# Optimization experiments

Measured on AMD Instinct MI355X. Metric: run time of the kernel, lower is better.

## Reference

```python
import jax, jax.numpy as jnp
import numpy as np

NUM_POINTS = 100000
BATCH = 4096
K = 10


def setup_inputs() -> dict:
    key = jax.random.key(0)
    k1, k2, k3, k4, k5 = jax.random.split(key, 5)
    rays_o = jax.random.normal(k1, (BATCH, 3), dtype=jnp.float32)
    rays_d = jax.random.normal(k2, (BATCH, 3), dtype=jnp.float32)
    xyz = jax.random.normal(k3, (NUM_POINTS, 3), dtype=jnp.float32) * 0.1
    features_dc = jax.random.normal(k4, (NUM_POINTS, 1, 3), dtype=jnp.float32)
    opacity = jax.random.normal(k5, (NUM_POINTS, 1), dtype=jnp.float32)
    return {"rays_o": rays_o, "rays_d": rays_d, "xyz": xyz,
            "features_dc": features_dc, "opacity": opacity}


def reference(rays_o, rays_d, xyz, features_dc, opacity):
    # colors = sigmoid(features[:,0,:]) ; features[:,0,:] == features_dc[:,0,:]
    colors = jax.nn.sigmoid(features_dc[:, 0, :])          # [N,3]
    op = jax.nn.sigmoid(opacity[:, 0])                      # [N]
    ray_centers = rays_o + rays_d * 3.0                     # [B,3]
    # Euclidean cdist via ||a||^2 + ||b||^2 - 2 a.b (matmul form, like torch.cdist p=2)
    sq = (jnp.sum(ray_centers * ray_centers, axis=1)[:, None]
          + jnp.sum(xyz * xyz, axis=1)[None, :]
          - 2.0 * ray_centers @ xyz.T)                      # [B,N]
    distances = jnp.sqrt(jnp.maximum(sq, 0.0))
    # top-K smallest distances per ray
    _, idx = jax.lax.top_k(-distances, K)                   # [B,K]
    d_sel = jnp.take_along_axis(distances, idx, axis=1)     # [B,K]
    w = jnp.exp(-d_sel * 0.1) * op[idx]                     # [B,K]
    w = w / (jnp.sum(w, axis=1, keepdims=True) + 1e-8)
    rgb = jnp.einsum('bk,bkc->bc', w, colors[idx])          # [B,3]
    return rgb
```

## Files before the change

### kernel.cpp

```cpp
#include <hip/hip_runtime.h>
#include <math.h>

#define NPTS   100000
#define NRAYS  4096
#define KTOP   10
#define KMER   12
#define CAP    128
#define LCAP   12

#define PPAIR  2
#define SBLK   98
#define RCS    64
#define RPBS   (NRAYS / RCS)

#define TPAIR  4
#define NPART  64
#define TRAYS  4
#define TGRP   16

typedef float v2f __attribute__((ext_vector_type(2)));

static_assert(SBLK * 1024 >= NPTS, "scan covers all points");
static_assert(TGRP * 2048 <= NPTS, "theta sample within real points");

__device__ __forceinline__ float4 make_center(const float* __restrict__ ro,
                                              const float* __restrict__ rd,
                                              int ray, float w) {
    float ox = ro[3 * ray + 0], oy = ro[3 * ray + 1], oz = ro[3 * ray + 2];
    float dx = rd[3 * ray + 0], dy = rd[3 * ray + 1], dz = rd[3 * ray + 2];
    float cx, cy, cz;
    {
#pragma clang fp contract(off)
        cx = ox + dx * 3.0f;
        cy = oy + dy * 3.0f;
        cz = oz + dz * 3.0f;
    }
    return make_float4(cx, cy, cz, w);
}

__device__ __forceinline__ float sigm(float x) { return 1.0f / (1.0f + expf(-x)); }

__device__ __forceinline__ float rfl(float x) {
    return __int_as_float(__builtin_amdgcn_readfirstlane(__float_as_int(x)));
}

__device__ __forceinline__ v2f score2(v2f px, v2f py, v2f pz, v2f pw,
                                      v2f rx, v2f ry, v2f rz) {
    v2f t = __builtin_elementwise_fma(pz, rz, pw);
    t = __builtin_elementwise_fma(py, ry, t);
    return __builtin_elementwise_fma(px, rx, t);
}

__device__ __forceinline__ unsigned long long mkkey(float sc, int id, bool v) {
    unsigned u = __float_as_uint(sc);
    u = (u & 0x80000000u) ? ~u : (u | 0x80000000u);
    unsigned long long k = ((unsigned long long)u << 32) | (unsigned)(~id);
    return v ? k : 0ull;
}

__global__ __launch_bounds__(256, 3) void theta_kernel(const float* __restrict__ xyz,
                                                       const float* __restrict__ ro,
                                                       const float* __restrict__ rd,
                                                       float4* __restrict__ c4,
                                                       int* __restrict__ cnt) {
    __shared__ float4 rsh[TRAYS];
    __shared__ float  Msh[4][TRAYS][64];
    const int tid = threadIdx.x, wave = tid >> 6, lane = tid & 63;
    const int rbase = blockIdx.x * TRAYS;

    if (tid < TRAYS) rsh[tid] = make_center(ro, rd, rbase + tid, 0.0f);
    __syncthreads();

    float4 rr[TRAYS];
#pragma unroll
    for (int r = 0; r < TRAYS; ++r) rr[r] = rsh[r];

    v2f M[TRAYS];
#pragma unroll
    for (int r = 0; r < TRAYS; ++r) M[r] = (v2f){-INFINITY, -INFINITY};

    v2f pxA[TPAIR], pyA[TPAIR], pzA[TPAIR], pwA[TPAIR];
    v2f pxB[TPAIR], pyB[TPAIR], pzB[TPAIR], pwB[TPAIR];

    auto loadg = [&](v2f* PX, v2f* PY, v2f* PZ, v2f* PW, int g) {
        const int id0 = g * 2048 + wave * 512 + lane;
#pragma unroll
        for (int u = 0; u < TPAIR; ++u) {
            int ia = id0 + (2 * u) * 64, ib = id0 + (2 * u + 1) * 64;
            float xa = xyz[3 * ia + 0], ya = xyz[3 * ia + 1], za = xyz[3 * ia + 2];
            float xb = xyz[3 * ib + 0], yb = xyz[3 * ib + 1], zb = xyz[3 * ib + 2];
            PX[u] = (v2f){xa, xb}; PY[u] = (v2f){ya, yb}; PZ[u] = (v2f){za, zb};
            PW[u] = (v2f){-0.5f * fmaf(xa, xa, fmaf(ya, ya, za * za)),
                          -0.5f * fmaf(xb, xb, fmaf(yb, yb, zb * zb))};
        }
    };
    auto computeg = [&](const v2f* PX, const v2f* PY, const v2f* PZ, const v2f* PW) {
#pragma unroll
        for (int r = 0; r < TRAYS; ++r) {
            const v2f rx = (v2f){rr[r].x, rr[r].x};
            const v2f ry = (v2f){rr[r].y, rr[r].y};
            const v2f rz = (v2f){rr[r].z, rr[r].z};
            v2f m = M[r];
#pragma unroll
            for (int u = 0; u < TPAIR; ++u)
                m = __builtin_elementwise_max(m, score2(PX[u], PY[u], PZ[u], PW[u], rx, ry, rz));
            M[r] = m;
        }
    };

    loadg(pxA, pyA, pzA, pwA, 0);
#pragma unroll 1
    for (int g = 0; g < TGRP; g += 2) {
        loadg(pxB, pyB, pzB, pwB, g + 1);
        computeg(pxA, pyA, pzA, pwA);
        if (g + 2 < TGRP) loadg(pxA, pyA, pzA, pwA, g + 2);
        computeg(pxB, pyB, pzB, pwB);
    }

#pragma unroll
    for (int r = 0; r < TRAYS; ++r)
        Msh[wave][r][lane] = fmaxf(M[r].x, M[r].y);
    __syncthreads();

    if (tid < TRAYS) {
        float vs[KTOP];
#pragma unroll
        for (int j = 0; j < KTOP; ++j) vs[j] = -INFINITY;
#pragma unroll 1
        for (int p = 0; p < NPART; ++p) {
            float v = fmaxf(fmaxf(Msh[0][tid][p], Msh[1][tid][p]),
                            fmaxf(Msh[2][tid][p], Msh[3][tid][p]));
#pragma unroll
            for (int t = KTOP - 1; t >= 1; --t) {
                bool up = v > vs[t - 1], here = v > vs[t];
                vs[t] = up ? vs[t - 1] : (here ? v : vs[t]);
            }
            vs[0] = fmaxf(vs[0], v);
        }
        float4 c = rsh[tid];
        c.w = vs[KTOP - 1];
        c4[rbase + tid] = c;
        cnt[rbase + tid] = 0;
    }
}

__global__ __launch_bounds__(256, 6) void scan_kernel(const float* __restrict__ xyz,
                                                      const float4* __restrict__ c4,
                                                      int* __restrict__ cnt,
                                                      float2* __restrict__ cand) {
    __shared__ int    lcnt[RPBS];
    __shared__ float2 lbuf[RPBS][LCAP];
    const int pblk = blockIdx.x, rchunk = blockIdx.y;
    const int tid = threadIdx.x, wave = tid >> 6, lane = tid & 63;
    const int rbase = rchunk * RPBS;

    if (tid < RPBS) lcnt[tid] = 0;

    const int id0 = pblk * 1024 + wave * 256 + lane;
    v2f px[PPAIR], py[PPAIR], pz[PPAIR], pw[PPAIR];
#pragma unroll
    for (int u = 0; u < PPAIR; ++u) {
        int ia = id0 + (2 * u) * 64, ib = id0 + (2 * u + 1) * 64;
        bool va = ia < NPTS, vb = ib < NPTS;
        int ca = va ? ia : 0, cb = vb ? ib : 0;
        float xa = xyz[3 * ca + 0], ya = xyz[3 * ca + 1], za = xyz[3 * ca + 2];
        float xb = xyz[3 * cb + 0], yb = xyz[3 * cb + 1], zb = xyz[3 * cb + 2];
        px[u] = (v2f){xa, xb}; py[u] = (v2f){ya, yb}; pz[u] = (v2f){za, zb};
        pw[u] = (v2f){va ? -0.5f * fmaf(xa, xa, fmaf(ya, ya, za * za)) : -INFINITY,
                      vb ? -0.5f * fmaf(xb, xb, fmaf(yb, yb, zb * zb)) : -INFINITY};
    }
    __syncthreads();

    auto emit = [&](int r, float sc, int id) {
        int slot = atomicAdd(&lcnt[r], 1);
        float2 e = make_float2(sc, __int_as_float(id));
        if (slot < LCAP) lbuf[r][slot] = e;
        else {
            int gs = atomicAdd(&cnt[rbase + r], 1);
            if (gs < CAP) cand[((rbase + r) << 7) + gs] = e;
        }
    };

    auto do_ray = [&](int r, float cx, float cy, float cz, float th) {
        const v2f rx = (v2f){cx, cx}, ry = (v2f){cy, cy}, rz = (v2f){cz, cz};
        v2f t0 = score2(px[0], py[0], pz[0], pw[0], rx, ry, rz);
        v2f t1 = score2(px[1], py[1], pz[1], pw[1], rx, ry, rz);
        float hm = fmaxf(fmaxf(t0.x, t0.y), fmaxf(t1.x, t1.y));

        if (__ballot(hm >= th)) {
            if (t0.x >= th) emit(r, t0.x, id0 + 0 * 64);
            if (t0.y >= th) emit(r, t0.y, id0 + 1 * 64);
            if (t1.x >= th) emit(r, t1.x, id0 + 2 * 64);
            if (t1.y >= th) emit(r, t1.y, id0 + 3 * 64);
        }
    };

    float qx[4], qy[4], qz[4], qw[4];
    float nx[4], ny[4], nz[4], nw[4];
#pragma unroll
    for (int j = 0; j < 4; ++j) {
        float4 t = c4[rbase + j];
        qx[j] = rfl(t.x); qy[j] = rfl(t.y); qz[j] = rfl(t.z); qw[j] = rfl(t.w);
    }
#pragma unroll 1
    for (int rb = 0; rb < RPBS; rb += 4) {
        const bool more = (rb + 4 < RPBS);
        if (more) {
#pragma unroll
            for (int j = 0; j < 4; ++j) {
                float4 t = c4[rbase + rb + 4 + j];
                nx[j] = rfl(t.x); ny[j] = rfl(t.y); nz[j] = rfl(t.z); nw[j] = rfl(t.w);
            }
        }
#pragma unroll
        for (int j = 0; j < 4; ++j) do_ray(rb + j, qx[j], qy[j], qz[j], qw[j]);
        if (more) {
#pragma unroll
            for (int j = 0; j < 4; ++j) { qx[j] = nx[j]; qy[j] = ny[j]; qz[j] = nz[j]; qw[j] = nw[j]; }
        }
    }

    __syncthreads();
    if (tid < RPBS) {
        int n = lcnt[tid];
        n = n < LCAP ? n : LCAP;
        if (n > 0) {
            const int rayid = rbase + tid;
            int base = atomicAdd(&cnt[rayid], n);
            for (int j = 0; j < n; ++j) {
                int slot = base + j;
                if (slot < CAP) cand[(rayid << 7) + slot] = lbuf[tid][j];
            }
        }
    }
}

__global__ __launch_bounds__(256) void merge_kernel(const float* __restrict__ ro,
                                                    const float* __restrict__ rd,
                                                    const int* __restrict__ cnt,
                                                    const float2* __restrict__ cand,
                                                    const float* __restrict__ xyz,
                                                    const float* __restrict__ fdc,
                                                    const float* __restrict__ opac,
                                                    float* __restrict__ out) {
    const int wave = threadIdx.x >> 6, lane = threadIdx.x & 63;
    const int ray = blockIdx.x * 4 + wave;

    int n = cnt[ray];
    n = n < CAP ? n : CAP;

    const float2* cl = cand + (ray << 7);
    float2 e0 = cl[lane];
    float2 e1 = cl[64 + lane];
    int id0 = __float_as_int(e0.y), id1 = __float_as_int(e1.y);

    unsigned long long k0 = mkkey(e0.x, id0, lane < n);
    unsigned long long k1 = mkkey(e1.x, id1, lane + 64 < n);

    int sel = -1;
    unsigned long long kl = k0 > k1 ? k0 : k1;
#pragma unroll
    for (int j = 0; j < KMER; ++j) {
        unsigned long long m = kl;
#pragma unroll
        for (int off = 1; off < 64; off <<= 1) {
            unsigned long long o = __shfl_xor(m, off);
            m = m > o ? m : o;
        }
        bool win = (kl == m) && (m != 0ull);
        int wid = (k0 >= k1) ? id0 : id1;
        unsigned long long wmask = __ballot(win);
        int wl = __ffsll(wmask) - 1;
        int bid = __shfl(wid, wl & 63);
        if (m == 0ull) bid = -1;
        if (lane == j) sel = bid;
        if (win) {
            if (k0 >= k1) k0 = 0ull; else k1 = 0ull;
            kl = k0 > k1 ? k0 : k1;
        }
    }

    float ox = ro[3 * ray + 0], oy = ro[3 * ray + 1], oz = ro[3 * ray + 2];
    float dx = rd[3 * ray + 0], dy = rd[3 * ray + 1], dz = rd[3 * ray + 2];
    float cxf, cyf, czf;
    {
#pragma clang fp contract(off)
        cxf = ox + dx * 3.0f;
        cyf = oy + dy * 3.0f;
        czf = oz + dz * 3.0f;
    }
    double Cx = (double)cxf, Cy = (double)cyf, Cz = (double)czf;
    double cn = Cx * Cx + Cy * Cy + Cz * Cz;

    bool valid = (lane < KMER) && (sel >= 0);
    int pid = valid ? sel : 0;
    double X = (double)xyz[3 * pid + 0];
    double Y = (double)xyz[3 * pid + 1];
    double Z = (double)xyz[3 * pid + 2];
    double sq = valid ? (cn + (X * X + Y * Y + Z * Z) - 2.0 * (Cx * X + Cy * Y + Cz * Z))
                      : (double)INFINITY;
    int cid = valid ? sel : 0x7fffffff;

    int rank = 0;
#pragma unroll
    for (int k = 0; k < KMER; ++k) {
        double sk = __shfl(sq, k);
        int    ik = __shfl(cid, k);
        if ((sk < sq) || (sk == sq && ik < cid)) ++rank;
    }

    bool take = valid && (rank < KTOP);
    float w = 0.0f, rr = 0.0f, gg = 0.0f, bb = 0.0f;
    if (take) {
        float dd = sqrtf(fmaxf((float)sq, 0.0f));
        w  = expf(-0.1f * dd) * sigm(opac[pid]);
        rr = w * sigm(fdc[3 * pid + 0]);
        gg = w * sigm(fdc[3 * pid + 1]);
        bb = w * sigm(fdc[3 * pid + 2]);
    }
#pragma unroll
    for (int off = 1; off < 64; off <<= 1) {
        w  += __shfl_xor(w,  off);
        rr += __shfl_xor(rr, off);
        gg += __shfl_xor(gg, off);
        bb += __shfl_xor(bb, off);
    }
    if (lane == 0) {
        float inv = 1.0f / (w + 1e-8f);
        out[3 * ray + 0] = rr * inv;
        out[3 * ray + 1] = gg * inv;
        out[3 * ray + 2] = bb * inv;
    }
}

extern "C" void kernel_launch(void* const* d_in, const int* in_sizes, int n_in,
                              void* d_out, int out_size, void* d_ws, size_t ws_size,
                              hipStream_t stream) {
    const float* rays_o = (const float*)d_in[0];
    const float* rays_d = (const float*)d_in[1];
    const float* xyz    = (const float*)d_in[2];
    const float* fdc    = (const float*)d_in[3];
    const float* opac   = (const float*)d_in[4];
    float* out = (float*)d_out;

    char* w = (char*)d_ws;
    float4* c4   = (float4*)w;   w += (size_t)NRAYS * 16;
    int*    cnt  = (int*)w;      w += (size_t)NRAYS * 4;
    float2* cand = (float2*)w;

    theta_kernel<<<NRAYS / TRAYS, 256, 0, stream>>>(xyz, rays_o, rays_d, c4, cnt);
    scan_kernel<<<dim3(SBLK, RCS), 256, 0, stream>>>(xyz, c4, cnt, cand);
    merge_kernel<<<NRAYS / 4, 256, 0, stream>>>(rays_o, rays_d, cnt, cand, xyz, fdc, opac, out);
}
```

Before: 154.9 us.

## Replace brute-force point scan with uniform grid binning and per-cell AABB culling

Builds a 16x16x16 uniform grid over the points each call. Kernels count points per cell and record per-cell coordinate min/max with atomics, prefix-sum the counts, and scatter the points into cell-sorted float4 records with precomputed norms. The scan then assigns one wave per ray: it tests each cell's AABB against the theta-derived distance bound, merges passing z-runs into contiguous ranges, and scores only those points, replacing the previous full points-by-rays sweep. This trades the dense scan for several extra small kernel launches and contended atomics in dense cells, and falls back to a full scan when the run list overflows; the theta kernel also doubles rays per block.

New measurement: 346.3 us. +123.6%, slower.

```diff
diff --git a/kernel.cpp b/kernel.cpp
--- a/kernel.cpp
+++ b/kernel.cpp
@@ -1,26 +1,25 @@
 #include <hip/hip_runtime.h>
 #include <math.h>
 
-#define NPTS   100000
-#define NRAYS  4096
-#define KTOP   10
-#define KMER   12
-#define CAP    128
-#define LCAP   12
-
-#define PPAIR  2
-#define SBLK   98
-#define RCS    64
-#define RPBS   (NRAYS / RCS)
-
-#define TPAIR  4
-#define NPART  64
-#define TRAYS  4
-#define TGRP   16
+#define NPTS    100000
+#define NRAYS   4096
+#define KTOP    10
+#define KMER    12
+#define CAP     128
+
+#define GCELLS  4096
+#define NCOL    256
+#define RCAP    256
+#define DMARGIN 1e-3f
+
+#define TPAIR   4
+#define NPART   64
+#define TRAYS   8
+#define TGRP    16
 
 typedef float v2f __attribute__((ext_vector_type(2)));
-
-static_assert(SBLK * 1024 >= NPTS, "scan covers all points");
+typedef unsigned int u32;
+
 static_assert(TGRP * 2048 <= NPTS, "theta sample within real points");
 
 __device__ __forceinline__ float4 make_center(const float* __restrict__ ro,
@@ -58,15 +57,36 @@
     return v ? k : 0ull;
 }
 
-__global__ __launch_bounds__(256, 3) void theta_kernel(const float* __restrict__ xyz,
+__device__ __forceinline__ u32 enc(float f) {
+    u32 u = __float_as_uint(f);
+    return (u & 0x80000000u) ? ~u : (u | 0x80000000u);
+}
+__device__ __forceinline__ float dec(u32 e) {
+    u32 u = (e & 0x80000000u) ? (e & 0x7fffffffu) : ~e;
+    return __uint_as_float(u);
+}
+
+__device__ __forceinline__ int cellcoord(float x) {
+    int v = (int)floorf((x + 0.8f) * 10.0f);
+    return v < 0 ? 0 : (v > 15 ? 15 : v);
+}
+
+__global__ __launch_bounds__(256, 2) void theta_kernel(const float* __restrict__ xyz,
                                                        const float* __restrict__ ro,
                                                        const float* __restrict__ rd,
                                                        float4* __restrict__ c4,
-                                                       int* __restrict__ cnt) {
+                                                       int* __restrict__ cnt,
+                                                       u32* __restrict__ cellblk) {
     __shared__ float4 rsh[TRAYS];
     __shared__ float  Msh[4][TRAYS][64];
     const int tid = threadIdx.x, wave = tid >> 6, lane = tid & 63;
     const int rbase = blockIdx.x * TRAYS;
+
+    {
+        const int gid = blockIdx.x * 256 + tid;
+        if (gid < 28672)
+            cellblk[gid] = (gid >= 4096 && gid < 16384) ? 0xFFFFFFFFu : 0u;
+    }
 
     if (tid < TRAYS) rsh[tid] = make_center(ro, rd, rbase + tid, 0.0f);
     __syncthreads();
@@ -144,95 +164,148 @@
     }
 }
 
-__global__ __launch_bounds__(256, 6) void scan_kernel(const float* __restrict__ xyz,
-                                                      const float4* __restrict__ c4,
-                                                      int* __restrict__ cnt,
-                                                      float2* __restrict__ cand) {
-    __shared__ int    lcnt[RPBS];
-    __shared__ float2 lbuf[RPBS][LCAP];
-    const int pblk = blockIdx.x, rchunk = blockIdx.y;
+__global__ __launch_bounds__(256) void count_kernel(const float* __restrict__ xyz,
+                                                    u32* __restrict__ cellcnt,
+                                                    u32* __restrict__ minenc,
+                                                    u32* __restrict__ maxenc) {
+    const int i = blockIdx.x * 256 + threadIdx.x;
+    if (i >= NPTS) return;
+    float x = xyz[3 * i + 0], y = xyz[3 * i + 1], z = xyz[3 * i + 2];
+    int cid = (cellcoord(x) << 8) | (cellcoord(y) << 4) | cellcoord(z);
+    atomicAdd(&cellcnt[cid], 1u);
+    atomicMin(&minenc[cid], enc(x));          atomicMax(&maxenc[cid], enc(x));
+    atomicMin(&minenc[4096 + cid], enc(y));   atomicMax(&maxenc[4096 + cid], enc(y));
+    atomicMin(&minenc[8192 + cid], enc(z));   atomicMax(&maxenc[8192 + cid], enc(z));
+}
+
+__global__ __launch_bounds__(256) void prefix_kernel(const u32* __restrict__ cellcnt,
+                                                     u32* __restrict__ cellstart,
+                                                     u32* __restrict__ cursor) {
+    __shared__ u32 wsum[4];
     const int tid = threadIdx.x, wave = tid >> 6, lane = tid & 63;
-    const int rbase = rchunk * RPBS;
-
-    if (tid < RPBS) lcnt[tid] = 0;
-
-    const int id0 = pblk * 1024 + wave * 256 + lane;
-    v2f px[PPAIR], py[PPAIR], pz[PPAIR], pw[PPAIR];
-#pragma unroll
-    for (int u = 0; u < PPAIR; ++u) {
-        int ia = id0 + (2 * u) * 64, ib = id0 + (2 * u + 1) * 64;
-        bool va = ia < NPTS, vb = ib < NPTS;
-        int ca = va ? ia : 0, cb = vb ? ib : 0;
-        float xa = xyz[3 * ca + 0], ya = xyz[3 * ca + 1], za = xyz[3 * ca + 2];
-        float xb = xyz[3 * cb + 0], yb = xyz[3 * cb + 1], zb = xyz[3 * cb + 2];
-        px[u] = (v2f){xa, xb}; py[u] = (v2f){ya, yb}; pz[u] = (v2f){za, zb};
-        pw[u] = (v2f){va ? -0.5f * fmaf(xa, xa, fmaf(ya, ya, za * za)) : -INFINITY,
-                      vb ? -0.5f * fmaf(xb, xb, fmaf(yb, yb, zb * zb)) : -INFINITY};
-    }
-    __syncthreads();
-
-    auto emit = [&](int r, float sc, int id) {
-        int slot = atomicAdd(&lcnt[r], 1);
-        float2 e = make_float2(sc, __int_as_float(id));
-        if (slot < LCAP) lbuf[r][slot] = e;
-        else {
-            int gs = atomicAdd(&cnt[rbase + r], 1);
-            if (gs < CAP) cand[((rbase + r) << 7) + gs] = e;
-        }
-    };
-
-    auto do_ray = [&](int r, float cx, float cy, float cz, float th) {
-        const v2f rx = (v2f){cx, cx}, ry = (v2f){cy, cy}, rz = (v2f){cz, cz};
-        v2f t0 = score2(px[0], py[0], pz[0], pw[0], rx, ry, rz);
-        v2f t1 = score2(px[1], py[1], pz[1], pw[1], rx, ry, rz);
-        float hm = fmaxf(fmaxf(t0.x, t0.y), fmaxf(t1.x, t1.y));
-
-        if (__ballot(hm >= th)) {
-            if (t0.x >= th) emit(r, t0.x, id0 + 0 * 64);
-            if (t0.y >= th) emit(r, t0.y, id0 + 1 * 64);
-            if (t1.x >= th) emit(r, t1.x, id0 + 2 * 64);
-            if (t1.y >= th) emit(r, t1.y, id0 + 3 * 64);
-        }
-    };
-
-    float qx[4], qy[4], qz[4], qw[4];
-    float nx[4], ny[4], nz[4], nw[4];
-#pragma unroll
-    for (int j = 0; j < 4; ++j) {
-        float4 t = c4[rbase + j];
-        qx[j] = rfl(t.x); qy[j] = rfl(t.y); qz[j] = rfl(t.z); qw[j] = rfl(t.w);
-    }
+    const int base = tid * 16;
+    u32 loc[16]; u32 s = 0;
+#pragma unroll
+    for (int k = 0; k < 16; ++k) { loc[k] = cellcnt[base + k]; s += loc[k]; }
+    u32 v = s;
+#pragma unroll
+    for (int off = 1; off < 64; off <<= 1) {
+        u32 o = __shfl_up(v, off);
+        if (lane >= off) v += o;
+    }
+    if (lane == 63) wsum[wave] = v;
+    __syncthreads();
+    u32 woff = 0;
+    for (int w = 0; w < 4; ++w) if (w < wave) woff += wsum[w];
+    u32 run = woff + v - s;
+#pragma unroll
+    for (int k = 0; k < 16; ++k) {
+        cellstart[base + k] = run;
+        cursor[base + k] = run;
+        run += loc[k];
+    }
+    if (tid == 255) cellstart[4096] = run;
+}
+
+__global__ __launch_bounds__(256) void scatter_kernel(const float* __restrict__ xyz,
+                                                      const u32* __restrict__ minenc,
+                                                      const u32* __restrict__ maxenc,
+                                                      u32* __restrict__ cursor,
+                                                      float4* __restrict__ pts4,
+                                                      int* __restrict__ pid,
+                                                      float4* __restrict__ aabbA,
+                                                      float2* __restrict__ aabbB) {
+    const int i = blockIdx.x * 256 + threadIdx.x;
+    if (i < GCELLS) {
+        float lox = dec(minenc[i]),        loy = dec(minenc[4096 + i]);
+        float loz = dec(minenc[8192 + i]), hix = dec(maxenc[i]);
+        float hiy = dec(maxenc[4096 + i]), hiz = dec(maxenc[8192 + i]);
+        int dst = ((i & 15) << 8) | (i >> 4);
+        aabbA[dst] = make_float4(lox, loy, loz, hix);
+        aabbB[dst] = make_float2(hiy, hiz);
+    }
+    if (i < NPTS) {
+        float x = xyz[3 * i + 0], y = xyz[3 * i + 1], z = xyz[3 * i + 2];
+        int cid = (cellcoord(x) << 8) | (cellcoord(y) << 4) | cellcoord(z);
+        u32 dst = atomicAdd(&cursor[cid], 1u);
+        pts4[dst] = make_float4(x, y, z, -0.5f * fmaf(x, x, fmaf(y, y, z * z)));
+        pid[dst] = i;
+    }
+}
+
+__global__ __launch_bounds__(256) void scan_kernel(const float4* __restrict__ pts4,
+                                                   const int* __restrict__ pid,
+                                                   const float4* __restrict__ aabbA,
+                                                   const float2* __restrict__ aabbB,
+                                                   const u32* __restrict__ cellstart,
+                                                   const float4* __restrict__ c4,
+                                                   int* __restrict__ cnt,
+                                                   float2* __restrict__ cand) {
+    __shared__ u32    runS[4][RCAP], runE[4][RCAP];
+    __shared__ float2 lbuf[4][CAP];
+    __shared__ int    nrun[4], lcnt[4];
+    const int tid = threadIdx.x, w = tid >> 6, lane = tid & 63;
+    const int ray = blockIdx.x * 4 + w;
+
+    float4 q = c4[ray];
+    const float cx = rfl(q.x), cy = rfl(q.y), cz = rfl(q.z), th = rfl(q.w);
+    const float limit = fmaf(cx, cx, fmaf(cy, cy, cz * cz)) - 2.0f * th + DMARGIN;
+
+    if (lane == 0) { nrun[w] = 0; lcnt[w] = 0; }
+    __syncthreads();
+
 #pragma unroll 1
-    for (int rb = 0; rb < RPBS; rb += 4) {
-        const bool more = (rb + 4 < RPBS);
-        if (more) {
-#pragma unroll
-            for (int j = 0; j < 4; ++j) {
-                float4 t = c4[rbase + rb + 4 + j];
-                nx[j] = rfl(t.x); ny[j] = rfl(t.y); nz[j] = rfl(t.z); nw[j] = rfl(t.w);
+    for (int cc = 0; cc < 4; ++cc) {
+        const int col = lane + cc * 64;
+        const int colbase = col << 4;
+        u32 mask = 0;
+#pragma unroll 1
+        for (int iz = 0; iz < 16; ++iz) {
+            float4 A = aabbA[iz * 256 + col];
+            float2 B = aabbB[iz * 256 + col];
+            float dx = fmaxf(fmaxf(A.x - cx, cx - A.w), 0.0f);
+            float dy = fmaxf(fmaxf(A.y - cy, cy - B.x), 0.0f);
+            float dz = fmaxf(fmaxf(A.z - cz, cz - B.y), 0.0f);
+            float d2 = fmaf(dx, dx, fmaf(dy, dy, dz * dz));
+            mask |= (d2 <= limit) ? (1u << iz) : 0u;
+        }
+        while (mask) {
+            int lo = __ffs(mask) - 1;
+            u32 t = mask >> lo;
+            int len = __ffs(~t) - 1;
+            mask &= ~(((1u << len) - 1u) << lo);
+            u32 s = cellstart[colbase + lo];
+            u32 e = cellstart[colbase + lo + len];
+            if (e > s) {
+                int slot = atomicAdd(&nrun[w], 1);
+                if (slot < RCAP) { runS[w][slot] = s; runE[w][slot] = e; }
             }
         }
-#pragma unroll
-        for (int j = 0; j < 4; ++j) do_ray(rb + j, qx[j], qy[j], qz[j], qw[j]);
-        if (more) {
-#pragma unroll
-            for (int j = 0; j < 4; ++j) { qx[j] = nx[j]; qy[j] = ny[j]; qz[j] = nz[j]; qw[j] = nw[j]; }
-        }
-    }
-
-    __syncthreads();
-    if (tid < RPBS) {
-        int n = lcnt[tid];
-        n = n < LCAP ? n : LCAP;
-        if (n > 0) {
-            const int rayid = rbase + tid;
-            int base = atomicAdd(&cnt[rayid], n);
-            for (int j = 0; j < n; ++j) {
-                int slot = base + j;
-                if (slot < CAP) cand[(rayid << 7) + slot] = lbuf[tid][j];
+    }
+    __syncthreads();
+
+    int NR = nrun[w];
+    const bool fb = NR > RCAP;
+    if (fb) NR = 1;
+#pragma unroll 1
+    for (int ri = 0; ri < NR; ++ri) {
+        u32 s = fb ? 0u : runS[w][ri];
+        u32 e = fb ? (u32)NPTS : runE[w][ri];
+        for (u32 j = s + lane; j < e; j += 64) {
+            float4 p = pts4[j];
+            float sc = fmaf(p.x, cx, fmaf(p.y, cy, fmaf(p.z, cz, p.w)));
+            if (sc >= th) {
+                int slot = atomicAdd(&lcnt[w], 1);
+                if (slot < CAP) lbuf[w][slot] = make_float2(sc, __int_as_float(pid[j]));
             }
         }
     }
+    __syncthreads();
+
+    int n = lcnt[w];
+    int m = n < CAP ? n : CAP;
+    for (int j = lane; j < m; j += 64) cand[(ray << 7) + j] = lbuf[w][j];
+    if (lane == 0) cnt[ray] = n;
 }
 
 __global__ __launch_bounds__(256) void merge_kernel(const float* __restrict__ ro,
@@ -293,10 +366,10 @@
     double cn = Cx * Cx + Cy * Cy + Cz * Cz;
 
     bool valid = (lane < KMER) && (sel >= 0);
-    int pid = valid ? sel : 0;
-    double X = (double)xyz[3 * pid + 0];
-    double Y = (double)xyz[3 * pid + 1];
-    double Z = (double)xyz[3 * pid + 2];
+    int pidv = valid ? sel : 0;
+    double X = (double)xyz[3 * pidv + 0];
+    double Y = (double)xyz[3 * pidv + 1];
+    double Z = (double)xyz[3 * pidv + 2];
     double sq = valid ? (cn + (X * X + Y * Y + Z * Z) - 2.0 * (Cx * X + Cy * Y + Cz * Z))
                       : (double)INFINITY;
     int cid = valid ? sel : 0x7fffffff;
@@ -313,10 +386,10 @@
     float w = 0.0f, rr = 0.0f, gg = 0.0f, bb = 0.0f;
     if (take) {
         float dd = sqrtf(fmaxf((float)sq, 0.0f));
-        w  = expf(-0.1f * dd) * sigm(opac[pid]);
-        rr = w * sigm(fdc[3 * pid + 0]);
-        gg = w * sigm(fdc[3 * pid + 1]);
-        bb = w * sigm(fdc[3 * pid + 2]);
+        w  = expf(-0.1f * dd) * sigm(opac[pidv]);
+        rr = w * sigm(fdc[3 * pidv + 0]);
+        gg = w * sigm(fdc[3 * pidv + 1]);
+        bb = w * sigm(fdc[3 * pidv + 2]);
     }
 #pragma unroll
     for (int off = 1; off < 64; off <<= 1) {
@@ -343,12 +416,28 @@
     const float* opac   = (const float*)d_in[4];
     float* out = (float*)d_out;
 
-    char* w = (char*)d_ws;
-    float4* c4   = (float4*)w;   w += (size_t)NRAYS * 16;
-    int*    cnt  = (int*)w;      w += (size_t)NRAYS * 4;
-    float2* cand = (float2*)w;
-
-    theta_kernel<<<NRAYS / TRAYS, 256, 0, stream>>>(xyz, rays_o, rays_d, c4, cnt);
-    scan_kernel<<<dim3(SBLK, RCS), 256, 0, stream>>>(xyz, c4, cnt, cand);
+    char* p = (char*)d_ws;
+    float4* c4       = (float4*)p;  p += (size_t)NRAYS  * 16;
+    float4* aabbA    = (float4*)p;  p += (size_t)GCELLS * 16;
+    float4* pts4     = (float4*)p;  p += (size_t)(NPTS + 352) * 16;
+    float2* aabbB    = (float2*)p;  p += (size_t)GCELLS * 8;
+    float2* cand     = (float2*)p;  p += (size_t)NRAYS * CAP * 8;
+    u32*    cellblk  = (u32*)p;     p += (size_t)28672 * 4;
+    u32*    cellstart= (u32*)p;     p += (size_t)4112 * 4;
+    u32*    cursor   = (u32*)p;     p += (size_t)GCELLS * 4;
+    int*    cnt      = (int*)p;     p += (size_t)NRAYS * 4;
+    int*    pid      = (int*)p;     p += (size_t)(NPTS + 352) * 4;
+
+    u32* cellcnt = cellblk;
+    u32* minenc  = cellblk + 4096;
+    u32* maxenc  = cellblk + 16384;
+
+    const int PB = (NPTS + 255) / 256;
+
+    theta_kernel<<<NRAYS / TRAYS, 256, 0, stream>>>(xyz, rays_o, rays_d, c4, cnt, cellblk);
+    count_kernel<<<PB, 256, 0, stream>>>(xyz, cellcnt, minenc, maxenc);
+    prefix_kernel<<<1, 256, 0, stream>>>(cellcnt, cellstart, cursor);
+    scatter_kernel<<<PB, 256, 0, stream>>>(xyz, minenc, maxenc, cursor, pts4, pid, aabbA, aabbB);
+    scan_kernel<<<NRAYS / 4, 256, 0, stream>>>(pts4, pid, aabbA, aabbB, cellstart, c4, cnt, cand);
     merge_kernel<<<NRAYS / 4, 256, 0, stream>>>(rays_o, rays_d, cnt, cand, xyz, fdc, opac, out);
 }
```
